# Kernel tuning notes

Hardware: AMD Instinct MI355X
Metric: run time of the kernel (lower is better)

## Reference

```python
import jax, jax.numpy as jnp
import numpy as np

NUM_HEADS = 16

def setup_inputs() -> dict:
    key = jax.random.key(0)
    k1, k2, k3 = jax.random.split(key, 3)
    B, S, D = 4, 2048, 1024
    x = jax.random.normal(k1, (B, S, D), dtype=jnp.float32)
    w_qkv = jax.random.normal(k2, (D, 3 * D), dtype=jnp.float32) * (1.0 / np.sqrt(D))
    b_qkv = jnp.zeros((3 * D,), dtype=jnp.float32)
    w_out = jax.random.normal(k3, (D, D), dtype=jnp.float32) * (1.0 / np.sqrt(D))
    b_out = jnp.zeros((D,), dtype=jnp.float32)
    return {"x": x, "w_qkv": w_qkv, "b_qkv": b_qkv, "w_out": w_out, "b_out": b_out}

def reference(x, w_qkv, b_qkv, w_out, b_out):
    B, S, D = x.shape
    H = NUM_HEADS
    Dh = D // H
    # fused QKV projection: [B,S,3D]
    qkv = jnp.einsum('bsd,de->bse', x, w_qkv) + b_qkv
    q, k, v = jnp.split(qkv, 3, axis=-1)
    # separate heads -> [B,H,S,Dh]
    def heads(t):
        return t.reshape(B, S, H, Dh).transpose(0, 2, 1, 3)
    q, k, v = heads(q), heads(k), heads(v)
    # scaled dot-product attention (no mask, no dropout)
    scale = 1.0 / jnp.sqrt(jnp.asarray(Dh, dtype=x.dtype))
    attn = jnp.einsum('bhqd,bhkd->bhqk', q, k) * scale
    weights = jax.nn.softmax(attn, axis=-1)
    out = jnp.einsum('bhqk,bhkd->bhqd', weights, v)
    # combine heads -> [B,S,D], then output projection
    out = out.transpose(0, 2, 1, 3).reshape(B, S, D)
    return jnp.einsum('bsd,de->bse', out, w_out) + b_out
```

## Files before the change

### kernel.cpp

```cpp
#include <hip/hip_runtime.h>

typedef unsigned short u16;
typedef __attribute__((ext_vector_type(8))) short v8s;
typedef __attribute__((ext_vector_type(4))) short v4s;
typedef __attribute__((ext_vector_type(4))) float v4f;

#define MFMA32(a, b, c) __builtin_amdgcn_mfma_f32_16x16x32_bf16(a, b, c, 0, 0, 0)

#if __has_builtin(__builtin_amdgcn_mfma_f32_16x16x16bf16_1k)
static __device__ __forceinline__ v4f mfma16(v4s a, v4s b, v4f c) {
    return __builtin_amdgcn_mfma_f32_16x16x16bf16_1k(a, b, c, 0, 0, 0);
}
#else
static __device__ __forceinline__ v4f mfma16(v4s a, v4s b, v4f c) {
    v4s z = {0, 0, 0, 0};
    v8s a8 = __builtin_shufflevector(a, z, 0, 1, 2, 3, 4, 5, 6, 7);
    v8s b8 = __builtin_shufflevector(b, z, 0, 1, 2, 3, 4, 5, 6, 7);
    return MFMA32(a8, b8, c);
}
#endif

static __device__ __forceinline__ u16 f32_to_bf16(float f) {
    unsigned int u = __builtin_bit_cast(unsigned int, f);
    u += 0x7fffu + ((u >> 16) & 1u);
    return (u16)(u >> 16);
}
static __device__ __forceinline__ v8s cvt8(v4f lo, v4f hi) {
    v8s r;
#pragma unroll
    for (int i = 0; i < 4; i++) {
        r[i]     = (short)f32_to_bf16(lo[i]);
        r[i + 4] = (short)f32_to_bf16(hi[i]);
    }
    return r;
}

__global__ void cast_f32_bf16(const float* __restrict__ in,
                              u16* __restrict__ out, int n8) {
    const int i = blockIdx.x * blockDim.x + threadIdx.x;
    if (i < n8) {
        v4f lo = ((const v4f*)in)[2 * i];
        v4f hi = ((const v4f*)in)[2 * i + 1];
        ((v8s*)out)[i] = cvt8(lo, hi);
    }
}

__global__ void transpose_f32_bf16(const float* __restrict__ in,
                                   u16* __restrict__ out, int R, int C) {
    __shared__ u16 t[32][33];
    const int tid = threadIdx.x;
    const int tx = tid & 31, ty = tid >> 5;
    const int c0 = blockIdx.x * 32, r0 = blockIdx.y * 32;
#pragma unroll
    for (int i = 0; i < 32; i += 8)
        t[ty + i][tx] = f32_to_bf16(in[(size_t)(r0 + ty + i) * C + c0 + tx]);
    __syncthreads();
#pragma unroll
    for (int i = 0; i < 32; i += 8)
        out[(size_t)(c0 + ty + i) * R + r0 + tx] = t[tx][ty + i];
}

template <int AMODE, int CMODE>
__global__ __launch_bounds__(256)
void gemm_bt(const void* __restrict__ A, int lda,
             const u16* __restrict__ Bt, int ldb,
             const float* __restrict__ bias,
             void* __restrict__ Cq, u16* __restrict__ Kb, u16* __restrict__ VtG,
             int ldc, int K) {
    __shared__ __align__(16) u16 As[128 * 72];
    __shared__ __align__(16) u16 Bs[128 * 72];

    const int tid  = threadIdx.x;
    const int wid  = tid >> 6;
    const int lane = tid & 63;
    const int l15  = lane & 15;
    const int quad = lane >> 4;
    const int bm = blockIdx.y * 128;
    const int bn = blockIdx.x * 128;
    const int wm = (wid & 1) * 64;
    const int wn = (wid >> 1) * 64;

    const int sr = tid >> 3;
    const int sg = (tid & 7) * 8;

    const float* Af = (const float*)A;
    const u16*   Au = (const u16*)A;

    v4f acc[4][4];
#pragma unroll
    for (int i = 0; i < 4; i++)
#pragma unroll
        for (int j = 0; j < 4; j++) acc[i][j] = (v4f)0.f;

    for (int kb = 0; kb < K; kb += 64) {
        v8s a[4], b[4];
#pragma unroll
        for (int i = 0; i < 4; i++) {
            const int row = sr + i * 32;
            if (AMODE) {
                const float* p = Af + (size_t)(bm + row) * lda + kb + sg;
                a[i] = cvt8(*(const v4f*)p, *(const v4f*)(p + 4));
            } else {
                a[i] = *(const v8s*)(Au + (size_t)(bm + row) * lda + kb + sg);
            }
            b[i] = *(const v8s*)(Bt + (size_t)(bn + row) * ldb + kb + sg);
        }
        __syncthreads();
#pragma unroll
        for (int i = 0; i < 4; i++) {
            const int row = sr + i * 32;
            *(v8s*)&As[row * 72 + sg] = a[i];
            *(v8s*)&Bs[row * 72 + sg] = b[i];
        }
        __syncthreads();

        v8s af[2][4], bf[2][4];
#pragma unroll
        for (int ko = 0; ko < 2; ko++) {
#pragma unroll
            for (int mt = 0; mt < 4; mt++)
                af[ko][mt] = *(const v8s*)&As[(wm + mt * 16 + l15) * 72 + ko * 32 + quad * 8];
#pragma unroll
            for (int nt = 0; nt < 4; nt++)
                bf[ko][nt] = *(const v8s*)&Bs[(wn + nt * 16 + l15) * 72 + ko * 32 + quad * 8];
        }
#pragma unroll
        for (int ko = 0; ko < 2; ko++)
#pragma unroll
            for (int mt = 0; mt < 4; mt++)
#pragma unroll
                for (int nt = 0; nt < 4; nt++)
                    acc[mt][nt] = MFMA32(af[ko][mt], bf[ko][nt], acc[mt][nt]);
    }

#pragma unroll
    for (int nt = 0; nt < 4; nt++) {
        const int n = bn + wn + nt * 16 + l15;
        const float bv = bias[n];
#pragma unroll
        for (int mt = 0; mt < 4; mt++) {
#pragma unroll
            for (int r = 0; r < 4; r++) {
                const int m = bm + wm + mt * 16 + quad * 4 + r;
                const float val = acc[mt][nt][r] + bv;
                if (CMODE == 1) {
                    ((float*)Cq)[(size_t)m * ldc + n] = val;
                } else {
                    const u16 o = f32_to_bf16(val);
                    const int region = n >> 10, nl = n & 1023;
                    if (region == 0) {
                        ((u16*)Cq)[(size_t)m * 1024 + nl] = o;
                    } else if (region == 1) {
                        Kb[(size_t)m * 1024 + nl] = o;
                    } else {
                        const int h = nl >> 6, dh = nl & 63;
                        const int b = m >> 11, s = m & 2047;
                        VtG[((size_t)((b * 16 + h) * 64 + dh)) * 2048 + s] = o;
                    }
                }
            }
        }
    }
}

__global__ __launch_bounds__(256)
void attn_fused(u16* __restrict__ Qb, const u16* __restrict__ Kb,
                const u16* __restrict__ VtG) {
    __shared__ __align__(16) u16 Ks[64 * 72];
    __shared__ __align__(16) u16 Vs[64 * 72];

    const int tid  = threadIdx.x;
    const int wid  = tid >> 6;
    const int lane = tid & 63;
    const int l15  = lane & 15;
    const int quad = lane >> 4;
    const int qt = blockIdx.x;
    const int h  = blockIdx.y;
    const int bz = blockIdx.z;

    const size_t qbase = (size_t)bz * 2048 * 1024;
    const int q0 = qt * 128 + wid * 32;

    v8s aq[2][2];
#pragma unroll
    for (int qh = 0; qh < 2; qh++) {
        const u16* qrow = Qb + qbase + (size_t)(q0 + qh * 16 + l15) * 1024 + h * 64 + quad * 8;
        aq[qh][0] = *(const v8s*)qrow;
        aq[qh][1] = *(const v8s*)(qrow + 32);
    }

    float lrow[2] = {0.f, 0.f};
    v4f accO[2][4];
#pragma unroll
    for (int qh = 0; qh < 2; qh++)
#pragma unroll
        for (int c = 0; c < 4; c++) accO[qh][c] = (v4f)0.f;

    const int sr = tid >> 3;
    const int sg = (tid & 7) * 8;
    const float SC = 0.18033688f;

    const u16* kpb = Kb + qbase + h * 64;
    const u16* vpb = VtG + (size_t)((bz * 16 + h) * 64) * 2048;

    for (int kt = 0; kt < 32; kt++) {
        const v8s k0 = *(const v8s*)(kpb + (size_t)(kt * 64 + sr) * 1024 + sg);
        const v8s k1 = *(const v8s*)(kpb + (size_t)(kt * 64 + sr + 32) * 1024 + sg);
        const v8s v0 = *(const v8s*)(vpb + (size_t)sr * 2048 + kt * 64 + sg);
        const v8s v1 = *(const v8s*)(vpb + (size_t)(sr + 32) * 2048 + kt * 64 + sg);
        __syncthreads();
        *(v8s*)&Ks[sr * 72 + sg]        = k0;
        *(v8s*)&Ks[(sr + 32) * 72 + sg] = k1;
        *(v8s*)&Vs[sr * 72 + sg]        = v0;
        *(v8s*)&Vs[(sr + 32) * 72 + sg] = v1;
        __syncthreads();

#pragma unroll
        for (int kc = 0; kc < 4; kc++) {
            const v8s kf0 = *(const v8s*)&Ks[(kc * 16 + l15) * 72 + quad * 8];
            const v8s kf1 = *(const v8s*)&Ks[(kc * 16 + l15) * 72 + 32 + quad * 8];
            v4s vf[4];
#pragma unroll
            for (int c = 0; c < 4; c++)
                vf[c] = *(const v4s*)&Vs[(c * 16 + l15) * 72 + kc * 16 + quad * 4];

#pragma unroll
            for (int qh = 0; qh < 2; qh++) {
                v4f st = (v4f)0.f;
                st = MFMA32(kf0, aq[qh][0], st);
                st = MFMA32(kf1, aq[qh][1], st);
                v4s pk;
                float rs = 0.f;
#pragma unroll
                for (int r = 0; r < 4; r++) {
                    const float p = exp2f(st[r] * SC);
                    rs += p;
                    pk[r] = (short)f32_to_bf16(p);
                }
                lrow[qh] += rs;
#pragma unroll
                for (int c = 0; c < 4; c++)
                    accO[qh][c] = mfma16(vf[c], pk, accO[qh][c]);
            }
        }
    }

#pragma unroll
    for (int qh = 0; qh < 2; qh++) {
        lrow[qh] += __shfl_xor(lrow[qh], 16);
        lrow[qh] += __shfl_xor(lrow[qh], 32);
    }

#pragma unroll
    for (int qh = 0; qh < 2; qh++) {
        const int q = q0 + qh * 16 + l15;
        const float inv = 1.f / lrow[qh];
#pragma unroll
        for (int c = 0; c < 4; c++) {
            v4s o;
#pragma unroll
            for (int r = 0; r < 4; r++)
                o[r] = (short)f32_to_bf16(accO[qh][c][r] * inv);
            *(v4s*)&Qb[qbase + (size_t)q * 1024 + h * 64 + c * 16 + quad * 4] = o;
        }
    }
}

extern "C" void kernel_launch(void* const* d_in, const int* in_sizes, int n_in,
                              void* d_out, int out_size, void* d_ws, size_t ws_size,
                              hipStream_t stream) {
    (void)in_sizes; (void)n_in; (void)out_size;
    const float* x    = (const float*)d_in[0];
    const float* wqkv = (const float*)d_in[1];
    const float* bqkv = (const float*)d_in[2];
    const float* wout = (const float*)d_in[3];
    const float* bout = (const float*)d_in[4];
    float* outp = (float*)d_out;

    char* ws = (char*)d_ws;
    const size_t BIG  = 58720256;
    const size_t BIGX = 75497472;

    if (ws_size >= BIG || ws_size == 0) {
        u16* Qb    = (u16*)(ws);
        u16* Kb    = (u16*)(ws + 16777216);
        u16* VtG   = (u16*)(ws + 33554432);
        u16* wqkvT = (u16*)(ws + 50331648);
        u16* woutT = (u16*)(ws + 56623104);
        u16* xb    = (u16*)(ws + 58720256);

        transpose_f32_bf16<<<dim3(96, 32), 256, 0, stream>>>(wqkv, wqkvT, 1024, 3072);
        transpose_f32_bf16<<<dim3(32, 32), 256, 0, stream>>>(wout, woutT, 1024, 1024);
        if (ws_size >= BIGX) {
            cast_f32_bf16<<<4096, 256, 0, stream>>>(x, xb, 1048576);
            gemm_bt<0, 2><<<dim3(24, 64), 256, 0, stream>>>(
                xb, 1024, wqkvT, 1024, bqkv, Qb, Kb, VtG, 0, 1024);
        } else {
            gemm_bt<1, 2><<<dim3(24, 64), 256, 0, stream>>>(
                x, 1024, wqkvT, 1024, bqkv, Qb, Kb, VtG, 0, 1024);
        }
        attn_fused<<<dim3(16, 16, 4), 256, 0, stream>>>(Qb, Kb, VtG);
        gemm_bt<0, 1><<<dim3(8, 64), 256, 0, stream>>>(
            Qb, 1024, woutT, 1024, bout, outp, nullptr, nullptr, 1024, 1024);
    } else {
        u16* wqkvT = (u16*)(ws);
        u16* woutT = (u16*)(ws + 6291456);
        u16* Qb    = (u16*)(ws + 8388608);
        u16* Kb    = (u16*)(ws + 12582912);
        u16* VtG   = (u16*)(ws + 16777216);

        transpose_f32_bf16<<<dim3(96, 32), 256, 0, stream>>>(wqkv, wqkvT, 1024, 3072);
        transpose_f32_bf16<<<dim3(32, 32), 256, 0, stream>>>(wout, woutT, 1024, 1024);
        for (int b = 0; b < 4; b++) {
            const float* xb = x + (size_t)b * 2048 * 1024;
            float* ob = outp + (size_t)b * 2048 * 1024;
            gemm_bt<1, 2><<<dim3(24, 16), 256, 0, stream>>>(
                xb, 1024, wqkvT, 1024, bqkv, Qb, Kb, VtG, 0, 1024);
            attn_fused<<<dim3(16, 16, 1), 256, 0, stream>>>(Qb, Kb, VtG);
            gemm_bt<0, 1><<<dim3(8, 16), 256, 0, stream>>>(
                Qb, 1024, woutT, 1024, bout, ob, nullptr, nullptr, 1024, 1024);
        }
    }
}
```

Baseline: 347.7 us.

## Prefetch K/V tiles into registers, widen key tile, use packed bf16 convert

```diff
diff --git a/kernel.cpp b/kernel.cpp
--- a/kernel.cpp
+++ b/kernel.cpp
@@ -25,14 +25,29 @@
     u += 0x7fffu + ((u >> 16) & 1u);
     return (u16)(u >> 16);
 }
+
+#if __has_builtin(__builtin_amdgcn_cvt_pk_bf16_f32)
+typedef __attribute__((ext_vector_type(2))) __bf16 v2bf;
+static __device__ __forceinline__ int cvt_pk2(float a, float b) {
+    v2bf p = __builtin_amdgcn_cvt_pk_bf16_f32(a, b);
+    return __builtin_bit_cast(int, p);
+}
+#else
+static __device__ __forceinline__ int cvt_pk2(float a, float b) {
+    return (int)f32_to_bf16(a) | ((int)f32_to_bf16(b) << 16);
+}
+#endif
+static __device__ __forceinline__ v4s pack4(float a, float b, float c, float d) {
+    int lo = cvt_pk2(a, b), hi = cvt_pk2(c, d);
+    typedef __attribute__((ext_vector_type(2))) int v2i;
+    v2i p = {lo, hi};
+    return __builtin_bit_cast(v4s, p);
+}
 static __device__ __forceinline__ v8s cvt8(v4f lo, v4f hi) {
-    v8s r;
-#pragma unroll
-    for (int i = 0; i < 4; i++) {
-        r[i]     = (short)f32_to_bf16(lo[i]);
-        r[i + 4] = (short)f32_to_bf16(hi[i]);
-    }
-    return r;
+    typedef __attribute__((ext_vector_type(4))) int v4i;
+    v4i p = {cvt_pk2(lo[0], lo[1]), cvt_pk2(lo[2], lo[3]),
+             cvt_pk2(hi[0], hi[1]), cvt_pk2(hi[2], hi[3])};
+    return __builtin_bit_cast(v8s, p);
 }
 
 __global__ void cast_f32_bf16(const float* __restrict__ in,
@@ -166,8 +181,8 @@
 __global__ __launch_bounds__(256)
 void attn_fused(u16* __restrict__ Qb, const u16* __restrict__ Kb,
                 const u16* __restrict__ VtG) {
-    __shared__ __align__(16) u16 Ks[64 * 72];
-    __shared__ __align__(16) u16 Vs[64 * 72];
+    __shared__ __align__(16) u16 Ks[128 * 72];
+    __shared__ __align__(16) u16 Vs[64 * 136];
 
     const int tid  = threadIdx.x;
     const int wid  = tid >> 6;
@@ -196,48 +211,60 @@
 #pragma unroll
         for (int c = 0; c < 4; c++) accO[qh][c] = (v4f)0.f;
 
-    const int sr = tid >> 3;
-    const int sg = (tid & 7) * 8;
+    const int krow = tid >> 3;
+    const int kcol = (tid & 7) * 8;
+    const int vrow = tid >> 4;
+    const int vcol = (tid & 15) * 8;
     const float SC = 0.18033688f;
 
     const u16* kpb = Kb + qbase + h * 64;
     const u16* vpb = VtG + (size_t)((bz * 16 + h) * 64) * 2048;
 
-    for (int kt = 0; kt < 32; kt++) {
-        const v8s k0 = *(const v8s*)(kpb + (size_t)(kt * 64 + sr) * 1024 + sg);
-        const v8s k1 = *(const v8s*)(kpb + (size_t)(kt * 64 + sr + 32) * 1024 + sg);
-        const v8s v0 = *(const v8s*)(vpb + (size_t)sr * 2048 + kt * 64 + sg);
-        const v8s v1 = *(const v8s*)(vpb + (size_t)(sr + 32) * 2048 + kt * 64 + sg);
+    v8s kreg[4], vreg[4];
+#pragma unroll
+    for (int i = 0; i < 4; i++) {
+        kreg[i] = *(const v8s*)(kpb + (size_t)(krow + i * 32) * 1024 + kcol);
+        vreg[i] = *(const v8s*)(vpb + (size_t)(vrow + i * 16) * 2048 + vcol);
+    }
+
+    for (int kt = 0; kt < 16; kt++) {
         __syncthreads();
-        *(v8s*)&Ks[sr * 72 + sg]        = k0;
-        *(v8s*)&Ks[(sr + 32) * 72 + sg] = k1;
-        *(v8s*)&Vs[sr * 72 + sg]        = v0;
-        *(v8s*)&Vs[(sr + 32) * 72 + sg] = v1;
+#pragma unroll
+        for (int i = 0; i < 4; i++) {
+            *(v8s*)&Ks[(krow + i * 32) * 72 + kcol]  = kreg[i];
+            *(v8s*)&Vs[(vrow + i * 16) * 136 + vcol] = vreg[i];
+        }
         __syncthreads();
 
-#pragma unroll
-        for (int kc = 0; kc < 4; kc++) {
+        if (kt < 15) {
+            const int kn = (kt + 1) * 128;
+#pragma unroll
+            for (int i = 0; i < 4; i++) {
+                kreg[i] = *(const v8s*)(kpb + (size_t)(kn + krow + i * 32) * 1024 + kcol);
+                vreg[i] = *(const v8s*)(vpb + (size_t)(vrow + i * 16) * 2048 + kn + vcol);
+            }
+        }
+
+#pragma unroll
+        for (int kc = 0; kc < 8; kc++) {
             const v8s kf0 = *(const v8s*)&Ks[(kc * 16 + l15) * 72 + quad * 8];
             const v8s kf1 = *(const v8s*)&Ks[(kc * 16 + l15) * 72 + 32 + quad * 8];
             v4s vf[4];
 #pragma unroll
             for (int c = 0; c < 4; c++)
-                vf[c] = *(const v4s*)&Vs[(c * 16 + l15) * 72 + kc * 16 + quad * 4];
+                vf[c] = *(const v4s*)&Vs[(c * 16 + l15) * 136 + kc * 16 + quad * 4];
 
 #pragma unroll
             for (int qh = 0; qh < 2; qh++) {
                 v4f st = (v4f)0.f;
                 st = MFMA32(kf0, aq[qh][0], st);
                 st = MFMA32(kf1, aq[qh][1], st);
-                v4s pk;
-                float rs = 0.f;
-#pragma unroll
-                for (int r = 0; r < 4; r++) {
-                    const float p = exp2f(st[r] * SC);
-                    rs += p;
-                    pk[r] = (short)f32_to_bf16(p);
-                }
-                lrow[qh] += rs;
+                const float p0 = exp2f(st[0] * SC);
+                const float p1 = exp2f(st[1] * SC);
+                const float p2 = exp2f(st[2] * SC);
+                const float p3 = exp2f(st[3] * SC);
+                lrow[qh] += (p0 + p1) + (p2 + p3);
+                const v4s pk = pack4(p0, p1, p2, p3);
 #pragma unroll
                 for (int c = 0; c < 4; c++)
                     accO[qh][c] = mfma16(vf[c], pk, accO[qh][c]);
@@ -257,10 +284,8 @@
         const float inv = 1.f / lrow[qh];
 #pragma unroll
         for (int c = 0; c < 4; c++) {
-            v4s o;
-#pragma unroll
-            for (int r = 0; r < 4; r++)
-                o[r] = (short)f32_to_bf16(accO[qh][c][r] * inv);
+            const v4s o = pack4(accO[qh][c][0] * inv, accO[qh][c][1] * inv,
+                                accO[qh][c][2] * inv, accO[qh][c][3] * inv);
             *(v4s*)&Qb[qbase + (size_t)q * 1024 + h * 64 + c * 16 + quad * 4] = o;
         }
     }
```

New measurement: 358.8 us. 1.03x slower.
